# Kernel tuning notes

Measured on AMD Instinct MI355X. Metric: run time of the kernel, lower is better.

Reference implementation:

```python
import jax, jax.numpy as jnp
import numpy as np

B, S, D = 32, 1024, 512  # batch, seq_len, d_feat (= din = 2*dhid)

def setup_inputs() -> dict:
    key = jax.random.key(0)
    ks = jax.random.split(key, 8)
    x = jax.random.normal(ks[0], (B, S, D), dtype=jnp.float32)
    x_len = jax.random.randint(ks[1], (B,), 1, S + 1).astype(jnp.int32)
    w_score = jax.random.normal(ks[2], (D,), dtype=jnp.float32) * 0.02
    b_score = jnp.zeros((), dtype=jnp.float32)
    Wq = jax.random.normal(ks[3], (D, D), dtype=jnp.float32) * 0.02
    bq = jnp.zeros((D,), dtype=jnp.float32)
    Wk = jax.random.normal(ks[4], (D, D), dtype=jnp.float32) * 0.02
    bk = jnp.zeros((D,), dtype=jnp.float32)
    beta_raw = jax.random.uniform(ks[5], (1,), minval=-0.01, maxval=0.01, dtype=jnp.float32)
    return {"x": x, "x_len": x_len, "slot_idx": 0, "w_score": w_score, "b_score": b_score,
            "Wq": Wq, "bq": bq, "Wk": Wk, "bk": bk, "beta_raw": beta_raw}

def reference(x, x_len, slot_idx, w_score, b_score, Wq, bq, Wk, bk, beta_raw):
    # valid-position mask from per-sample lengths: [B, S]
    mask = jnp.arange(x.shape[1])[None, :] < x_len[:, None]
    neg_inf = jnp.float32(-jnp.inf)

    # ---- local branch: linear scorer -> masked softmax -> weighted sum ----
    local_scores = jnp.einsum('bsd,d->bs', x, w_score) + b_score          # [B, S]
    local_scores = jnp.where(mask, local_scores, neg_inf)
    local_w = jax.nn.softmax(local_scores, axis=1)
    c_local = jnp.einsum('bs,bsd->bd', local_w, x)                        # [B, D]

    # ---- global branch: QK bmm -> row-sum -> masked softmax -> weighted sum of x ----
    q = jnp.einsum('bsd,de->bse', x, Wq) + bq                             # [B, S, D]
    k = jnp.einsum('bsd,de->bse', x, Wk) + bk                             # [B, S, D]
    attn = jnp.einsum('bid,bjd->bij', q, k) / jnp.sqrt(jnp.float32(x.shape[2]))  # [B, S, S]
    g_scores = attn.sum(axis=2)                                           # [B, S] (sum over ALL j, as in source)
    g_scores = jnp.where(mask, g_scores, neg_inf)
    g_w = jax.nn.softmax(g_scores, axis=1)
    c_global = jnp.einsum('bs,bsd->bd', g_w, x)                           # [B, D]

    # ---- beta-weighted combination ----
    beta = jax.nn.sigmoid(beta_raw[slot_idx])
    c = c_local * beta + c_global * (1.0 - beta)
    return (x, c)
```

## Files before the change

kernel.cpp:

```cpp
#include <hip/hip_runtime.h>
#include <float.h>
#include <math.h>

#define BB 32
#define SS 1024
#define DD 512
#define NCH 32
#define CROWS 32
#define RW 8
#define NXCH 16

typedef float f32x4 __attribute__((ext_vector_type(4)));
typedef float f32x2 __attribute__((ext_vector_type(2)));

__device__ __forceinline__ float wave_reduce_add(float v) {
    #pragma unroll
    for (int m = 32; m >= 1; m >>= 1) v += __shfl_xor(v, m, 64);
    return v;
}

__global__ __launch_bounds__(256) void k_xsumx(
    const float* __restrict__ x, float* __restrict__ xsum_part)
{
    int sc = blockIdx.x, b = blockIdx.y, tid = threadIdx.x;
    const float* xb = x + ((size_t)b * SS + sc * 64) * DD + tid * 2;
    f32x2 acc = {0.f, 0.f};
    #pragma unroll 8
    for (int r = 0; r < 64; ++r)
        acc += *(const f32x2*)(xb + (size_t)r * DD);
    *(f32x2*)(xsum_part + ((size_t)b * NXCH + sc) * DD + tid * 2) = acc;
}

__global__ __launch_bounds__(256) void k_ks(
    const float* __restrict__ xsum_part, const float* __restrict__ Wk,
    float* __restrict__ ks_part)
{
    __shared__ float xs[8][64];
    int dc = blockIdx.x, eb = blockIdx.y, bg = blockIdx.z;
    int tid = threadIdx.x;
    int e = eb * 256 + tid;
    #pragma unroll
    for (int k = 0; k < 2; ++k) {
        int i = tid + k * 256;
        int bi = i >> 6, dl = i & 63;
        int b = bg * 8 + bi, d = dc * 64 + dl;
        float v = 0.f;
        #pragma unroll
        for (int scc = 0; scc < NXCH; ++scc)
            v += xsum_part[((size_t)b * NXCH + scc) * DD + d];
        xs[bi][dl] = v;
    }
    __syncthreads();
    float acc[8] = {0,0,0,0,0,0,0,0};
    #pragma unroll 8
    for (int dl = 0; dl < 64; ++dl) {
        float w = Wk[(size_t)(dc * 64 + dl) * DD + e];
        #pragma unroll
        for (int bi = 0; bi < 8; ++bi) acc[bi] += xs[bi][dl] * w;
    }
    #pragma unroll
    for (int bi = 0; bi < 8; ++bi) {
        int b = bg * 8 + bi;
        ks_part[((size_t)dc * BB + b) * DD + e] = acc[bi];
    }
}

__global__ __launch_bounds__(256) void k_v(
    const float* __restrict__ ks_part, const float* __restrict__ Wq,
    const float* __restrict__ bk, float* __restrict__ v_part)
{
    __shared__ float wq_lds[256 * 65];
    __shared__ float ks_lds[8][64];
    int ec = blockIdx.x, db = blockIdx.y, bg = blockIdx.z;
    int tid = threadIdx.x;
    #pragma unroll
    for (int k = 0; k < 2; ++k) {
        int i = tid + k * 256;
        int bi = i >> 6, el = i & 63;
        int b = bg * 8 + bi, e = ec * 64 + el;
        float val = (float)SS * bk[e];
        #pragma unroll
        for (int dcc = 0; dcc < 8; ++dcc)
            val += ks_part[((size_t)dcc * BB + b) * DD + e];
        ks_lds[bi][el] = val;
    }
    #pragma unroll
    for (int it = 0; it < 16; ++it) {
        int idx = tid + it * 256;
        int rowd = idx >> 4, col4 = idx & 15;
        f32x4 wv = *(const f32x4*)(Wq + (size_t)(db * 256 + rowd) * DD + ec * 64 + col4 * 4);
        float* dst = &wq_lds[rowd * 65 + col4 * 4];
        dst[0] = wv.x; dst[1] = wv.y; dst[2] = wv.z; dst[3] = wv.w;
    }
    __syncthreads();
    float acc[8] = {0,0,0,0,0,0,0,0};
    #pragma unroll 8
    for (int el = 0; el < 64; ++el) {
        float wq = wq_lds[tid * 65 + el];
        #pragma unroll
        for (int bi = 0; bi < 8; ++bi) acc[bi] += ks_lds[bi][el] * wq;
    }
    int d = db * 256 + tid;
    #pragma unroll
    for (int bi = 0; bi < 8; ++bi) {
        int b = bg * 8 + bi;
        v_part[((size_t)ec * BB + b) * DD + d] = acc[bi];
    }
}

__global__ __launch_bounds__(256) void k_pass1full(
    const float* __restrict__ x, const float* __restrict__ w_score,
    const float* __restrict__ v_part, const int* __restrict__ x_len,
    float* __restrict__ out_x,
    float* __restrict__ lP, float* __restrict__ lm, float* __restrict__ lS,
    float* __restrict__ gP, float* __restrict__ gm, float* __restrict__ gS)
{
    __shared__ float v_lds[DD];
    __shared__ float red_l[4][DD];
    __shared__ float red_g[4][DD];
    __shared__ float msl[4], Ssl[4], msg[4], Ssg[4];
    int b = blockIdx.x, sc = blockIdx.y;
    int wave = threadIdx.x >> 6, lane = threadIdx.x & 63, tid = threadIdx.x;
    int len = x_len[b];
    int s0 = sc * CROWS + wave * RW;
    size_t base = ((size_t)b * SS + s0) * DD;

    #pragma unroll
    for (int i = 0; i < 2; ++i) {
        int d = tid + i * 256;
        float vv = 0.f;
        #pragma unroll
        for (int ec = 0; ec < 8; ++ec) vv += v_part[((size_t)ec * BB + b) * DD + d];
        v_lds[d] = vv;
    }
    __syncthreads();
    const f32x4* vr = (const f32x4*)v_lds;
    f32x4 v0 = vr[lane], v1 = vr[lane + 64];
    const f32x4* wr = (const f32x4*)w_score;
    f32x4 w0 = wr[lane], w1 = wr[lane + 64];

    f32x4 a[RW][2];
    #pragma unroll
    for (int r = 0; r < RW; ++r) {
        const f32x4* xr = (const f32x4*)(x + base + (size_t)r * DD);
        a[r][0] = xr[lane];
        a[r][1] = xr[lane + 64];
    }
    #pragma unroll
    for (int r = 0; r < RW; ++r) {
        f32x4* orow = (f32x4*)(out_x + base + (size_t)r * DD);
        __builtin_nontemporal_store(a[r][0], &orow[lane]);
        __builtin_nontemporal_store(a[r][1], &orow[lane + 64]);
    }
    float pl[RW], pg[RW];
    #pragma unroll
    for (int r = 0; r < RW; ++r) {
        f32x4 t0 = a[r][0] * w0 + a[r][1] * w1;
        pl[r] = t0.x + t0.y + t0.z + t0.w;
        f32x4 u0 = a[r][0] * v0 + a[r][1] * v1;
        pg[r] = u0.x + u0.y + u0.z + u0.w;
    }
    #pragma unroll
    for (int r = 0; r < RW; ++r) {
        pl[r] = wave_reduce_add(pl[r]);
        pg[r] = wave_reduce_add(pg[r]) * 0.04419417382415922f;
    }
    float mwl = -FLT_MAX, mwg = -FLT_MAX;
    #pragma unroll
    for (int r = 0; r < RW; ++r) {
        if (s0 + r < len) {
            mwl = fmaxf(mwl, pl[r]);
            mwg = fmaxf(mwg, pg[r]);
        }
    }
    float Swl = 0.f, Swg = 0.f;
    f32x4 cl0 = {0,0,0,0}, cl1 = {0,0,0,0}, cg0 = {0,0,0,0}, cg1 = {0,0,0,0};
    #pragma unroll
    for (int r = 0; r < RW; ++r) {
        bool valid = (s0 + r) < len;
        float wl = valid ? __expf(pl[r] - mwl) : 0.f;
        float wg = valid ? __expf(pg[r] - mwg) : 0.f;
        Swl += wl; Swg += wg;
        cl0 += wl * a[r][0]; cl1 += wl * a[r][1];
        cg0 += wg * a[r][0]; cg1 += wg * a[r][1];
    }
    f32x4* rl = (f32x4*)red_l[wave];
    f32x4* rg = (f32x4*)red_g[wave];
    rl[lane] = cl0; rl[lane + 64] = cl1;
    rg[lane] = cg0; rg[lane + 64] = cg1;
    if (lane == 0) { msl[wave] = mwl; Ssl[wave] = Swl; msg[wave] = mwg; Ssg[wave] = Swg; }
    __syncthreads();
    float mcl = fmaxf(fmaxf(msl[0], msl[1]), fmaxf(msl[2], msl[3]));
    float mcg = fmaxf(fmaxf(msg[0], msg[1]), fmaxf(msg[2], msg[3]));
    float el0 = __expf(msl[0] - mcl), el1 = __expf(msl[1] - mcl);
    float el2 = __expf(msl[2] - mcl), el3 = __expf(msl[3] - mcl);
    float eg0 = __expf(msg[0] - mcg), eg1 = __expf(msg[1] - mcg);
    float eg2 = __expf(msg[2] - mcg), eg3 = __expf(msg[3] - mcg);
    #pragma unroll
    for (int i = 0; i < 2; ++i) {
        int d = tid + i * 256;
        size_t off = ((size_t)b * NCH + sc) * DD + d;
        lP[off] = red_l[0][d]*el0 + red_l[1][d]*el1 + red_l[2][d]*el2 + red_l[3][d]*el3;
        gP[off] = red_g[0][d]*eg0 + red_g[1][d]*eg1 + red_g[2][d]*eg2 + red_g[3][d]*eg3;
    }
    if (tid == 0) {
        lm[b * NCH + sc] = mcl;
        lS[b * NCH + sc] = Ssl[0]*el0 + Ssl[1]*el1 + Ssl[2]*el2 + Ssl[3]*el3;
        gm[b * NCH + sc] = mcg;
        gS[b * NCH + sc] = Ssg[0]*eg0 + Ssg[1]*eg1 + Ssg[2]*eg2 + Ssg[3]*eg3;
    }
}

__global__ __launch_bounds__(512) void k_combine(
    const float* __restrict__ lP, const float* __restrict__ lm, const float* __restrict__ lS,
    const float* __restrict__ gP, const float* __restrict__ gm, const float* __restrict__ gS,
    const int* __restrict__ slot_idx, const float* __restrict__ beta_raw,
    float* __restrict__ out_c)
{
    int b = blockIdx.x, d = threadIdx.x;
    float Ml = -FLT_MAX, Mg = -FLT_MAX;
    #pragma unroll 8
    for (int c = 0; c < NCH; ++c) {
        Ml = fmaxf(Ml, lm[b * NCH + c]);
        Mg = fmaxf(Mg, gm[b * NCH + c]);
    }
    float Sl = 0.f, Pl = 0.f, Sg = 0.f, Pg = 0.f;
    #pragma unroll 4
    for (int c = 0; c < NCH; ++c) {
        float wl = __expf(lm[b * NCH + c] - Ml);
        float wg = __expf(gm[b * NCH + c] - Mg);
        Sl += lS[b * NCH + c] * wl;
        Sg += gS[b * NCH + c] * wg;
        Pl += lP[((size_t)b * NCH + c) * DD + d] * wl;
        Pg += gP[((size_t)b * NCH + c) * DD + d] * wg;
    }
    float br = beta_raw[slot_idx[0]];
    float beta = 1.f / (1.f + __expf(-br));
    out_c[b * DD + d] = beta * Pl / Sl + (1.f - beta) * Pg / Sg;
}

extern "C" void kernel_launch(void* const* d_in, const int* in_sizes, int n_in,
                              void* d_out, int out_size, void* d_ws, size_t ws_size,
                              hipStream_t stream) {
    const float* x        = (const float*)d_in[0];
    const int*   x_len    = (const int*)d_in[1];
    const int*   slot_idx = (const int*)d_in[2];
    const float* w_score  = (const float*)d_in[3];
    const float* Wq       = (const float*)d_in[5];
    const float* Wk       = (const float*)d_in[7];
    const float* bk       = (const float*)d_in[8];
    const float* beta_raw = (const float*)d_in[9];

    float* out   = (float*)d_out;
    float* out_x = out;
    float* out_c = out + (size_t)BB * SS * DD;

    float* ws = (float*)d_ws;
    float* xsum_part = ws;
    float* ks_part   = ws + 262144;
    float* v_part    = ws + 393216;
    float* lP        = ws + 524288;
    float* gP        = ws + 1048576;
    float* lm        = ws + 1572864;
    float* lS        = ws + 1573888;
    float* gm        = ws + 1574912;
    float* gS        = ws + 1575936;

    k_xsumx<<<dim3(NXCH, BB), 256, 0, stream>>>(x, xsum_part);
    k_ks<<<dim3(8, 2, 4), 256, 0, stream>>>(xsum_part, Wk, ks_part);
    k_v<<<dim3(8, 2, 4), 256, 0, stream>>>(ks_part, Wq, bk, v_part);
    k_pass1full<<<dim3(BB, NCH), 256, 0, stream>>>(x, w_score, v_part, x_len, out_x,
                                                   lP, lm, lS, gP, gm, gS);
    k_combine<<<BB, 512, 0, stream>>>(lP, lm, lS, gP, gm, gS, slot_idx, beta_raw, out_c);
}
```

Before: 57.49 us.

## Move x copy from the final pass into the column-sum kernel

The copy of x to the output buffer moves out of the main scoring pass and into the first kernel, which already streams all of x to compute partial column sums. The first kernel now reads float4 vectors and writes 32 partial sums per batch instead of 16, and workspace offsets are rearranged to fit the larger buffer. The aim is to spread the 64MB write traffic into an earlier kernel and make the scoring pass purely read-bound. Total traffic is unchanged, so the gain depends on the first kernel absorbing the writes better than the later pass did.

```diff
diff --git a/kernel.cpp b/kernel.cpp
--- a/kernel.cpp
+++ b/kernel.cpp
@@ -8,10 +8,9 @@
 #define NCH 32
 #define CROWS 32
 #define RW 8
-#define NXCH 16
+#define NXCH 32
 
 typedef float f32x4 __attribute__((ext_vector_type(4)));
-typedef float f32x2 __attribute__((ext_vector_type(2)));
 
 __device__ __forceinline__ float wave_reduce_add(float v) {
     #pragma unroll
@@ -19,16 +18,21 @@
     return v;
 }
 
-__global__ __launch_bounds__(256) void k_xsumx(
-    const float* __restrict__ x, float* __restrict__ xsum_part)
-{
-    int sc = blockIdx.x, b = blockIdx.y, tid = threadIdx.x;
-    const float* xb = x + ((size_t)b * SS + sc * 64) * DD + tid * 2;
-    f32x2 acc = {0.f, 0.f};
-    #pragma unroll 8
-    for (int r = 0; r < 64; ++r)
-        acc += *(const f32x2*)(xb + (size_t)r * DD);
-    *(f32x2*)(xsum_part + ((size_t)b * NXCH + sc) * DD + tid * 2) = acc;
+__global__ __launch_bounds__(256) void k_copyxsum(
+    const float* __restrict__ x, float* __restrict__ out_x,
+    float* __restrict__ xsum_part)
+{
+    int ch = blockIdx.x, b = blockIdx.y, tid = threadIdx.x;
+    int p = tid >> 7, col4 = (tid & 127) * 4;
+    size_t base = ((size_t)b * SS + ch * 64 + p) * DD + col4;
+    f32x4 acc = {0.f, 0.f, 0.f, 0.f};
+    #pragma unroll 8
+    for (int it = 0; it < 32; ++it) {
+        const f32x4 v = *(const f32x4*)(x + base + (size_t)it * 2 * DD);
+        __builtin_nontemporal_store(v, (f32x4*)(out_x + base + (size_t)it * 2 * DD));
+        acc += v;
+    }
+    *(f32x4*)(xsum_part + ((size_t)b * NXCH + ch * 2 + p) * DD + col4) = acc;
 }
 
 __global__ __launch_bounds__(256) void k_ks(
@@ -45,7 +49,7 @@
         int bi = i >> 6, dl = i & 63;
         int b = bg * 8 + bi, d = dc * 64 + dl;
         float v = 0.f;
-        #pragma unroll
+        #pragma unroll 8
         for (int scc = 0; scc < NXCH; ++scc)
             v += xsum_part[((size_t)b * NXCH + scc) * DD + d];
         xs[bi][dl] = v;
@@ -108,10 +112,9 @@
     }
 }
 
-__global__ __launch_bounds__(256) void k_pass1full(
+__global__ __launch_bounds__(256) void k_pass2both(
     const float* __restrict__ x, const float* __restrict__ w_score,
     const float* __restrict__ v_part, const int* __restrict__ x_len,
-    float* __restrict__ out_x,
     float* __restrict__ lP, float* __restrict__ lm, float* __restrict__ lS,
     float* __restrict__ gP, float* __restrict__ gm, float* __restrict__ gS)
 {
@@ -145,12 +148,6 @@
         const f32x4* xr = (const f32x4*)(x + base + (size_t)r * DD);
         a[r][0] = xr[lane];
         a[r][1] = xr[lane + 64];
-    }
-    #pragma unroll
-    for (int r = 0; r < RW; ++r) {
-        f32x4* orow = (f32x4*)(out_x + base + (size_t)r * DD);
-        __builtin_nontemporal_store(a[r][0], &orow[lane]);
-        __builtin_nontemporal_store(a[r][1], &orow[lane + 64]);
     }
     float pl[RW], pg[RW];
     #pragma unroll
@@ -257,19 +254,19 @@
 
     float* ws = (float*)d_ws;
     float* xsum_part = ws;
-    float* ks_part   = ws + 262144;
-    float* v_part    = ws + 393216;
     float* lP        = ws + 524288;
     float* gP        = ws + 1048576;
-    float* lm        = ws + 1572864;
-    float* lS        = ws + 1573888;
-    float* gm        = ws + 1574912;
-    float* gS        = ws + 1575936;
-
-    k_xsumx<<<dim3(NXCH, BB), 256, 0, stream>>>(x, xsum_part);
+    float* ks_part   = ws + 1572864;
+    float* v_part    = ws + 1703936;
+    float* lm        = ws + 1835008;
+    float* lS        = ws + 1836032;
+    float* gm        = ws + 1837056;
+    float* gS        = ws + 1838080;
+
+    k_copyxsum<<<dim3(16, BB), 256, 0, stream>>>(x, out_x, xsum_part);
     k_ks<<<dim3(8, 2, 4), 256, 0, stream>>>(xsum_part, Wk, ks_part);
     k_v<<<dim3(8, 2, 4), 256, 0, stream>>>(ks_part, Wq, bk, v_part);
-    k_pass1full<<<dim3(BB, NCH), 256, 0, stream>>>(x, w_score, v_part, x_len, out_x,
+    k_pass2both<<<dim3(BB, NCH), 256, 0, stream>>>(x, w_score, v_part, x_len,
                                                    lP, lm, lS, gP, gm, gS);
     k_combine<<<BB, 512, 0, stream>>>(lP, lm, lS, gP, gm, gS, slot_idx, beta_raw, out_c);
 }
```

Result: slower. 60.26 us (+4.8%).
